# Kernel tuning notes

Measured on AMD Instinct MI355X. Metric: run time of the kernel, lower is better.

The kernel has to match this reference:

```python
import jax, jax.numpy as jnp
import numpy as np

G = 2.0  # gamma divergence parameter (obj='importance', g != 1.0 -> log_g path)

def setup_inputs() -> dict:
    key = jax.random.key(0)
    ks = jax.random.split(key, 6)
    V, H, N, K = 250000, 128, 32768, 256
    weight = jax.random.normal(ks[0], (V, H), dtype=jnp.float32) * 0.02
    bias = jax.random.normal(ks[1], (V,), dtype=jnp.float32) * 0.02
    hiddens = jax.random.normal(ks[2], (N, H), dtype=jnp.float32)
    # Categorical(noise).logits: normalized log-probabilities over the vocab
    noise_logits = jax.nn.log_softmax(jax.random.normal(ks[3], (V,), dtype=jnp.float32))
    targets = jax.random.randint(ks[4], (N,), 0, V, dtype=jnp.int64)
    samples = jax.random.randint(ks[5], (K,), 0, V, dtype=jnp.int64)
    return {"weight": weight, "bias": bias, "hiddens": hiddens,
            "noise_logits": noise_logits, "targets": targets, "samples": samples}

def reference(weight, bias, hiddens, noise_logits, targets, samples):
    N = hiddens.shape[0]
    K = samples.shape[0]
    # target score: <h_i, w_{t_i}> + b_{t_i}  -> [N]
    target_model = jnp.sum(hiddens * weight[targets], axis=1) + bias[targets]
    # noise scores: small gathered-weight GEMM -> [N, K]
    noise_model = hiddens @ weight[samples].T + bias[samples]
    model_logits = jnp.concatenate([target_model[:, None], noise_model], axis=1)  # [N, K+1]
    noise_l = jnp.concatenate(
        [noise_logits[targets][:, None],
         jnp.broadcast_to(noise_logits[samples][None, :], (N, K))], axis=1)
    output = model_logits - noise_l  # [N, K+1]
    # log_g: logits - log(sum(exp(g*logits)))/g, computed stably via logsumexp
    res0 = output[:, 0] - jax.nn.logsumexp(G * output, axis=1) / G  # new_targets are all 0
    return -jnp.sum(res0) / N
```

## Files before the change

kernel.cpp:

```cpp
#include <hip/hip_runtime.h>
#include <hip/hip_bf16.h>

typedef unsigned short u16;
typedef __attribute__((ext_vector_type(4))) float f32x4;
typedef __attribute__((ext_vector_type(8))) short bf16x8;

#define HDIM 128

__device__ __forceinline__ short f2b(float x) {
  union { __hip_bfloat16 b; short s; } u;
  u.b = __float2bfloat16(x);
  return u.s;
}

__global__ void prep_kernel(const float* __restrict__ weight,
                            const float* __restrict__ bias,
                            const float* __restrict__ nlog,
                            const int* __restrict__ samples,
                            u16* __restrict__ wsb,
                            float* __restrict__ ck2,
                            float* __restrict__ acc) {
  const int k = blockIdx.x;
  const int s = samples[k];
  wsb[k * HDIM + threadIdx.x] = (u16)f2b(weight[(size_t)s * HDIM + threadIdx.x]);
  if (threadIdx.x == 0) {
    ck2[k] = 2.0f * (bias[s] - nlog[s]);
    if (k == 0) acc[0] = 0.0f;
  }
}

__launch_bounds__(256, 2)
__global__ void loss_kernel(const float* __restrict__ hiddens,
                            const float* __restrict__ weight,
                            const float* __restrict__ bias,
                            const float* __restrict__ nlog,
                            const int* __restrict__ targets,
                            const u16* __restrict__ wsb,
                            const float* __restrict__ ck2,
                            float* __restrict__ acc) {
  __shared__ float sc[64 * 256];
  const int tid  = threadIdx.x;
  const int lane = tid & 63;
  const int wave = tid >> 6;
  const int m    = lane & 15;
  const int quad = lane >> 4;
  const int wrow = wave * 16;
  const int row  = blockIdx.x * 64 + wrow + m;

  const float* __restrict__ hrow = hiddens + (size_t)row * HDIM;

  const int tgt = targets[row];
  const float* __restrict__ trow = weight + (size_t)tgt * HDIM;
  float p = 0.0f;
#pragma unroll
  for (int j = 0; j < 8; ++j) {
    const float4 hv = *reinterpret_cast<const float4*>(hrow + quad * 32 + j * 4);
    const float4 wv = *reinterpret_cast<const float4*>(trow + quad * 32 + j * 4);
    p += hv.x * wv.x + hv.y * wv.y + hv.z * wv.z + hv.w * wv.w;
  }
  p += __shfl_xor(p, 16);
  p += __shfl_xor(p, 32);
  const float y0 = 2.0f * (p + bias[tgt] - nlog[tgt]);

  bf16x8 af[4];
#pragma unroll
  for (int kq = 0; kq < 4; ++kq) {
    const float4 f0 = *reinterpret_cast<const float4*>(hrow + kq * 32 + quad * 8);
    const float4 f1 = *reinterpret_cast<const float4*>(hrow + kq * 32 + quad * 8 + 4);
    bf16x8 a;
    a[0] = f2b(f0.x); a[1] = f2b(f0.y); a[2] = f2b(f0.z); a[3] = f2b(f0.w);
    a[4] = f2b(f1.x); a[5] = f2b(f1.y); a[6] = f2b(f1.z); a[7] = f2b(f1.w);
    af[kq] = a;
  }

#pragma unroll 4
  for (int ct = 0; ct < 16; ++ct) {
    const int col = ct * 16 + m;
    const u16* __restrict__ bp = wsb + (size_t)col * HDIM;
    f32x4 c = {0.f, 0.f, 0.f, 0.f};
#pragma unroll
    for (int kq = 0; kq < 4; ++kq) {
      const bf16x8 bf = *reinterpret_cast<const bf16x8*>(bp + kq * 32 + quad * 8);
      c = __builtin_amdgcn_mfma_f32_16x16x32_bf16(af[kq], bf, c, 0, 0, 0);
    }
    const float ckv = ck2[col];
#pragma unroll
    for (int r = 0; r < 4; ++r) {
      const int rl = quad * 4 + r;
      const int cs = col ^ ((rl & 7) << 2);
      sc[(wrow + rl) * 256 + cs] = 2.0f * c[r] + ckv;
    }
  }
  __syncthreads();

  const int roff = (wrow + m) * 256 + quad * 64;
  const int rot  = (m + quad * 16) & 63;
  float s = 0.0f;
#pragma unroll 16
  for (int j = 0; j < 64; ++j) {
    const float v = sc[roff + ((j + rot) & 63)];
    s += __expf(v - y0);
  }
  s += __shfl_xor(s, 16);
  s += __shfl_xor(s, 32);
  float res0 = -0.5f * __logf(s + 1.0f);
  res0 += __shfl_xor(res0, 1);
  res0 += __shfl_xor(res0, 2);
  res0 += __shfl_xor(res0, 4);
  res0 += __shfl_xor(res0, 8);
  if (lane == 0) atomicAdd(acc, res0);
}

__global__ void finish_kernel(const float* __restrict__ acc,
                              float* __restrict__ out, float scale) {
  out[0] = acc[0] * scale;
}

extern "C" void kernel_launch(void* const* d_in, const int* in_sizes, int n_in,
                              void* d_out, int out_size, void* d_ws, size_t ws_size,
                              hipStream_t stream) {
  const float* weight  = (const float*)d_in[0];
  const float* bias    = (const float*)d_in[1];
  const float* hiddens = (const float*)d_in[2];
  const float* nlog    = (const float*)d_in[3];
  const int*   targets = (const int*)d_in[4];
  const int*   samples = (const int*)d_in[5];
  const int N = in_sizes[2] / HDIM;
  const int K = in_sizes[5];

  u16*   wsb = (u16*)d_ws;
  float* ck2 = (float*)((char*)d_ws + (size_t)K * HDIM * sizeof(u16));
  float* acc = ck2 + K;

  prep_kernel<<<K, HDIM, 0, stream>>>(weight, bias, nlog, samples, wsb, ck2, acc);
  loss_kernel<<<N / 64, 256, 0, stream>>>(hiddens, weight, bias, nlog, targets,
                                          wsb, ck2, acc);
  finish_kernel<<<1, 1, 0, stream>>>(acc, (float*)d_out, -1.0f / (float)N);
}
```

Baseline: 219.0 us.

## Fuse exp-sum epilogue into MFMA loop, removing shared-memory score staging

Instead of writing the 64x256 score tile to LDS, syncing, and re-reading it for the exp-sum, each lane now applies exp directly to its MFMA accumulator values and keeps per-row partial sums, reduced afterwards with shuffles. The factor of 2 is folded into the bf16 sample weights during prep. Dropping the 64KB LDS buffer allows raising launch bounds to 4 blocks per CU. The cost is extra cross-lane shuffle reductions and broadcasting y0 per output row.

New measurement: 222.4 us. Within noise of the previous version (+1.5%).

```diff
diff --git a/kernel.cpp b/kernel.cpp
--- a/kernel.cpp
+++ b/kernel.cpp
@@ -22,14 +22,15 @@
                             float* __restrict__ acc) {
   const int k = blockIdx.x;
   const int s = samples[k];
-  wsb[k * HDIM + threadIdx.x] = (u16)f2b(weight[(size_t)s * HDIM + threadIdx.x]);
+  wsb[k * HDIM + threadIdx.x] =
+      (u16)f2b(2.0f * weight[(size_t)s * HDIM + threadIdx.x]);
   if (threadIdx.x == 0) {
     ck2[k] = 2.0f * (bias[s] - nlog[s]);
     if (k == 0) acc[0] = 0.0f;
   }
 }
 
-__launch_bounds__(256, 2)
+__launch_bounds__(256, 4)
 __global__ void loss_kernel(const float* __restrict__ hiddens,
                             const float* __restrict__ weight,
                             const float* __restrict__ bias,
@@ -38,14 +39,12 @@
                             const u16* __restrict__ wsb,
                             const float* __restrict__ ck2,
                             float* __restrict__ acc) {
-  __shared__ float sc[64 * 256];
   const int tid  = threadIdx.x;
   const int lane = tid & 63;
   const int wave = tid >> 6;
   const int m    = lane & 15;
   const int quad = lane >> 4;
-  const int wrow = wave * 16;
-  const int row  = blockIdx.x * 64 + wrow + m;
+  const int row  = blockIdx.x * 64 + wave * 16 + m;
 
   const float* __restrict__ hrow = hiddens + (size_t)row * HDIM;
 
@@ -62,6 +61,10 @@
   p += __shfl_xor(p, 32);
   const float y0 = 2.0f * (p + bias[tgt] - nlog[tgt]);
 
+  float y0r[4];
+#pragma unroll
+  for (int r = 0; r < 4; ++r) y0r[r] = __shfl(y0, quad * 4 + r);
+
   bf16x8 af[4];
 #pragma unroll
   for (int kq = 0; kq < 4; ++kq) {
@@ -73,6 +76,7 @@
     af[kq] = a;
   }
 
+  float s0 = 0.f, s1 = 0.f, s2 = 0.f, s3 = 0.f;
 #pragma unroll 4
   for (int ct = 0; ct < 16; ++ct) {
     const int col = ct * 16 + m;
@@ -83,32 +87,26 @@
       const bf16x8 bf = *reinterpret_cast<const bf16x8*>(bp + kq * 32 + quad * 8);
       c = __builtin_amdgcn_mfma_f32_16x16x32_bf16(af[kq], bf, c, 0, 0, 0);
     }
-    const float ckv = ck2[col];
+    const float e = ck2[col];
+    s0 += __expf(c[0] + e - y0r[0]);
+    s1 += __expf(c[1] + e - y0r[1]);
+    s2 += __expf(c[2] + e - y0r[2]);
+    s3 += __expf(c[3] + e - y0r[3]);
+  }
+
 #pragma unroll
-    for (int r = 0; r < 4; ++r) {
-      const int rl = quad * 4 + r;
-      const int cs = col ^ ((rl & 7) << 2);
-      sc[(wrow + rl) * 256 + cs] = 2.0f * c[r] + ckv;
-    }
+  for (int d = 1; d < 16; d <<= 1) {
+    s0 += __shfl_xor(s0, d);
+    s1 += __shfl_xor(s1, d);
+    s2 += __shfl_xor(s2, d);
+    s3 += __shfl_xor(s3, d);
   }
-  __syncthreads();
-
-  const int roff = (wrow + m) * 256 + quad * 64;
-  const int rot  = (m + quad * 16) & 63;
-  float s = 0.0f;
-#pragma unroll 16
-  for (int j = 0; j < 64; ++j) {
-    const float v = sc[roff + ((j + rot) & 63)];
-    s += __expf(v - y0);
-  }
-  s += __shfl_xor(s, 16);
-  s += __shfl_xor(s, 32);
-  float res0 = -0.5f * __logf(s + 1.0f);
-  res0 += __shfl_xor(res0, 1);
-  res0 += __shfl_xor(res0, 2);
-  res0 += __shfl_xor(res0, 4);
-  res0 += __shfl_xor(res0, 8);
-  if (lane == 0) atomicAdd(acc, res0);
+  float part = __logf(1.0f + s0) + __logf(1.0f + s1) +
+               __logf(1.0f + s2) + __logf(1.0f + s3);
+  part *= -0.5f;
+  part += __shfl_xor(part, 16);
+  part += __shfl_xor(part, 32);
+  if (lane == 0) atomicAdd(acc, part);
 }
 
 __global__ void finish_kernel(const float* __restrict__ acc,
```
